# Kernel optimization log

Measured on AMD Instinct MI355X. Metric: run time of the kernel, lower is better.

Reference implementation:

```python
import jax, jax.numpy as jnp
import numpy as np

NUM_NODES = 50000
NUM_RELS = 256
D = 256            # node_in_feat
TEXT_D = 256       # text_emb_dim
T_TOTAL = 24       # number of unique timestep graphs
E = 20000          # edges per timestep graph
B = 16             # batch of query times
SEQ_LEN = 7


def setup_inputs() -> dict:
    key = jax.random.key(0)
    ks = jax.random.split(key, 12)
    s = 1.0 / np.sqrt(D)
    return {
        "node_embeds": jax.random.normal(ks[0], (NUM_NODES, D), jnp.float32),
        "text_emb": jax.random.normal(ks[1], (T_TOTAL, E, TEXT_D), jnp.float32),
        "text_w_W": jax.random.uniform(ks[2], (TEXT_D, D), jnp.float32, -s, s),
        "text_w_b": jax.random.uniform(ks[3], (D,), jnp.float32, -s, s),
        "edge_w_W": jax.random.uniform(ks[4], (3 * D, D), jnp.float32, -s, s),
        "edge_w_b": jax.random.uniform(ks[5], (D,), jnp.float32, -s, s),
        "gru_Wih": jax.random.uniform(ks[6], (D, 3 * D), jnp.float32, -s, s),
        "gru_Whh": jax.random.uniform(ks[7], (D, 3 * D), jnp.float32, -s, s),
        "gru_bih": jax.random.uniform(ks[8], (3 * D,), jnp.float32, -s, s),
        "gru_bhh": jax.random.uniform(ks[9], (3 * D,), jnp.float32, -s, s),
        "edge_src": jax.random.randint(ks[10], (T_TOTAL, E), 0, NUM_NODES, jnp.int32),
        "edge_dst": jax.random.randint(jax.random.fold_in(ks[10], 1), (T_TOTAL, E), 0, NUM_NODES, jnp.int32),
        "edge_rel": jax.random.randint(jax.random.fold_in(ks[10], 2), (T_TOTAL, E), 0, NUM_RELS, jnp.int32),
        "time_idx": jax.random.randint(ks[11], (B, SEQ_LEN), 0, T_TOTAL, jnp.int32),
    }


def _gru(seqs, Wih, Whh, bih, bhh):
    # seqs: [B, R, S, d] -> run GRU over S, return final hidden [B, R, d]
    xs = jnp.moveaxis(seqs, 2, 0)  # [S, B, R, d]
    h0 = jnp.zeros(seqs.shape[:2] + (seqs.shape[-1],), seqs.dtype)

    def step(h, x):
        gi = x @ Wih + bih            # [B, R, 3d]
        gh = h @ Whh + bhh
        i_r, i_z, i_n = jnp.split(gi, 3, axis=-1)
        h_r, h_z, h_n = jnp.split(gh, 3, axis=-1)
        r = jax.nn.sigmoid(i_r + h_r)
        z = jax.nn.sigmoid(i_z + h_z)
        n = jnp.tanh(i_n + r * h_n)
        h_new = (1.0 - z) * n + z * h
        return h_new, None

    h_final, _ = jax.lax.scan(step, h0, xs)
    return h_final


def reference(node_embeds, text_emb, text_w_W, text_w_b, edge_w_W, edge_w_b,
              gru_Wih, gru_Whh, gru_bih, gru_bhh,
              edge_src, edge_dst, edge_rel, time_idx):
    # edge text projection (text_w): [T, E, D]
    text_h = text_emb @ text_w_W + text_w_b
    # gather node embeddings per edge endpoint
    h_src = node_embeds[edge_src]  # [T, E, D]
    h_dst = node_embeds[edge_dst]  # [T, E, D]
    # concat + edge MLP + ReLU: e_h = relu(edge_w([src || text || dst]))
    e = jnp.concatenate([h_src, text_h, h_dst], axis=-1)  # [T, E, 3D]
    e_h = jax.nn.relu(e @ edge_w_W + edge_w_b)            # [T, E, D]

    # scatter-mean of edge embeddings by relation type per timestep graph;
    # relations absent in a graph get zeros (init_rel_embeds = zeros)
    seg = lambda v, r: jax.ops.segment_sum(v, r, num_segments=NUM_RELS)
    sums = jax.vmap(seg)(e_h, edge_rel)                               # [T, R, D]
    counts = jax.vmap(seg)(jnp.ones(edge_rel.shape, e_h.dtype), edge_rel)  # [T, R]
    counts = counts[..., None]
    rel_emb = jnp.where(counts > 0, sums / jnp.maximum(counts, 1.0), 0.0)  # [T, R, D]

    # per query time: gather its window of timestep rel-embeddings and run
    # the GRU over time (relations act as the GRU batch dim, like transpose(0,1))
    seqs = rel_emb[time_idx]                 # [B, S, R, D]
    seqs = jnp.swapaxes(seqs, 1, 2)          # [B, R, S, D]
    hn = _gru(seqs, gru_Wih, gru_Whh, gru_bih, gru_bhh)  # [B, R, D]
    return hn
```

## Files before the change

### kernel.cpp

```cpp
#include <hip/hip_runtime.h>
#include <cstdint>
#include <cstddef>

#define NNODES 50000
#define NPAD   50048
#define NRELS  256
#define DIM    256
#define TT     24
#define EE     20000
#define BATCH  16
#define SEQQ   7

typedef __bf16 bf16;
typedef __bf16 bf16x4 __attribute__((ext_vector_type(4)));
typedef __bf16 bf16x8 __attribute__((ext_vector_type(8)));
typedef float  f32x4  __attribute__((ext_vector_type(4)));

__device__ __forceinline__ void gload16(const void* g, void* l){
  __builtin_amdgcn_global_load_lds((const __attribute__((address_space(1))) void*)g,
                                   (__attribute__((address_space(3))) void*)l, 16, 0, 0);
}


__global__ void k_cvt8(const float* __restrict__ in, bf16* __restrict__ out, int n8){
  int i = blockIdx.x*256 + threadIdx.x;
  if (i >= n8) return;
  const float4* p = (const float4*)in + (size_t)i*2;
  float4 a = p[0], b = p[1];
  bf16x8 o;
  o[0]=(bf16)a.x; o[1]=(bf16)a.y; o[2]=(bf16)a.z; o[3]=(bf16)a.w;
  o[4]=(bf16)b.x; o[5]=(bf16)b.y; o[6]=(bf16)b.z; o[7]=(bf16)b.w;
  ((bf16x8*)out)[i] = o;
}

__global__ void k_build_wbt(const float* __restrict__ tW, const float* __restrict__ eW,
                            bf16* __restrict__ WbT){
  int n = blockIdx.x, j = threadIdx.x;
  WbT[(size_t)n*768 + j]       = (bf16)eW[(size_t)j*256 + n];
  WbT[(size_t)n*768 + 512 + j] = (bf16)eW[(size_t)(512+j)*256 + n];
  float acc = 0.f;
  for (int m=0; m<256; ++m) acc += tW[(size_t)j*256 + m] * eW[(size_t)(256+m)*256 + n];
  WbT[(size_t)n*768 + 256 + j] = (bf16)acc;
}

__global__ void k_bias(const float* __restrict__ tb, const float* __restrict__ eW,
                       const float* __restrict__ eb, float* __restrict__ bf){
  int n = threadIdx.x;
  float acc = eb[n];
  for (int m=0; m<256; ++m) acc += tb[m] * eW[(size_t)(256+m)*256 + n];
  bf[n] = acc;
}

__global__ void k_gruWT(const float* __restrict__ W, bf16* __restrict__ WT){
  int n = blockIdx.x, k = threadIdx.x;
  WT[(size_t)n*256 + k] = (bf16)W[(size_t)k*768 + n];
}

__global__ void k_hist(const int* __restrict__ rel, int* __restrict__ counts,
                       int* __restrict__ offs, int* __restrict__ cursor){
  __shared__ int hist[256];
  __shared__ int scan[256];
  int t = blockIdx.x, tid = threadIdx.x;
  hist[tid] = 0;
  __syncthreads();
  for (int e = tid; e < EE; e += 256) atomicAdd(&hist[rel[(size_t)t*EE + e]], 1);
  __syncthreads();
  int v = hist[tid];
  scan[tid] = v;
  __syncthreads();
  for (int d=1; d<256; d<<=1){
    int add = (tid >= d) ? scan[tid-d] : 0;
    __syncthreads();
    scan[tid] += add;
    __syncthreads();
  }
  int ex = scan[tid] - v;
  counts[t*256+tid] = v;
  offs[t*256+tid]   = ex;
  cursor[t*256+tid] = ex;
}

__global__ void k_perm(const int* __restrict__ rel, const int* __restrict__ esrc,
                       const int* __restrict__ edst, int* __restrict__ cursor,
                       int* __restrict__ gperm, int* __restrict__ src_p,
                       int* __restrict__ dst_p){
  int t = blockIdx.y;
  int e = blockIdx.x*256 + threadIdx.x;
  if (e < EE){
    int r = rel[(size_t)t*EE + e];
    int p = atomicAdd(&cursor[t*256 + r], 1);
    size_t g = (size_t)t*EE + p;
    gperm[g] = t*EE + e;
    src_p[g] = esrc[(size_t)t*EE + e];
    dst_p[g] = edst[(size_t)t*EE + e];
  }
}

__global__ __launch_bounds__(256) void k_projn(
    const bf16* __restrict__ Abf, const bf16* __restrict__ WbT, int koff,
    bf16* __restrict__ out)
{
  int m0 = blockIdx.x*128;
  int tid = threadIdx.x, lane = tid&63, w = tid>>6;
  int l15 = lane&15, lq = lane>>4;
  int c0 = w*64;
  __shared__ __align__(16) bf16 Al[128*32];
  __shared__ __align__(16) bf16 Bl[256*32];

  f32x4 acc[8][4];
  f32x4 z4 = {0.f,0.f,0.f,0.f};
  #pragma unroll
  for (int mi=0;mi<8;++mi)
    #pragma unroll
    for (int ni=0;ni<4;++ni) acc[mi][ni]=z4;

  for (int ks=0; ks<8; ++ks){
    int k0 = ks*32;
    #pragma unroll
    for (int p=0;p<2;++p){
      int c = p*256 + tid;
      int rw = c>>2, prt = c&3;
      int pp = prt ^ ((rw>>1)&3);
      const char* src = (const char*)(Abf + (size_t)(m0+rw)*256 + k0) + pp*16;
      gload16(src, (char*)Al + (size_t)(p*256 + w*64)*16);
    }
    #pragma unroll
    for (int p=0;p<4;++p){
      int c = p*256 + tid;
      int nn = c>>2, prt = c&3;
      int pp = prt ^ ((nn>>1)&3);
      const char* src = (const char*)(WbT + (size_t)nn*768 + koff + k0) + pp*16;
      gload16(src, (char*)Bl + (size_t)(p*256 + w*64)*16);
    }
    __syncthreads();
    bf16x8 b[4];
    #pragma unroll
    for (int ni=0;ni<4;++ni){
      int nn = c0 + ni*16 + l15;
      b[ni] = *(const bf16x8*)((const char*)Bl + (size_t)nn*64 + (size_t)((lq ^ ((nn>>1)&3))*16));
    }
    #pragma unroll
    for (int mi=0;mi<8;++mi){
      int rw = mi*16 + l15;
      bf16x8 a = *(const bf16x8*)((const char*)Al + (size_t)rw*64 + (size_t)((lq ^ ((rw>>1)&3))*16));
      #pragma unroll
      for (int ni=0;ni<4;++ni)
        acc[mi][ni] = __builtin_amdgcn_mfma_f32_16x16x32_bf16(b[ni], a, acc[mi][ni], 0,0,0);
    }
    __syncthreads();
  }
  #pragma unroll
  for (int mi=0;mi<8;++mi){
    int row = m0 + mi*16 + l15;
    #pragma unroll
    for (int ni=0;ni<4;++ni){
      bf16x4 o;
      #pragma unroll
      for (int q=0;q<4;++q) o[q] = (bf16)acc[mi][ni][q];
      *(bf16x4*)(out + (size_t)row*256 + c0 + ni*16 + lq*4) = o;
    }
  }
}

__global__ __launch_bounds__(256,4) void k_projt(
    const float* __restrict__ text, const int* __restrict__ gperm,
    const bf16* __restrict__ WbT, bf16* __restrict__ out)
{
  int m0 = blockIdx.x*64;
  int tid = threadIdx.x, lane = tid&63, w = tid>>6;
  int l15 = lane&15, lq = lane>>4;
  int c0 = w*64;
  __shared__ __align__(16) bf16 Al[64*32];
  __shared__ __align__(16) bf16 Bl[256*32];

  int r0 = tid>>2;
  int part = tid&3;
  int pp0 = part ^ ((r0>>1)&3);
  const float* aP0 = text + (size_t)gperm[m0 + r0]*256;

  f32x4 acc[4][4];
  f32x4 z4 = {0.f,0.f,0.f,0.f};
  #pragma unroll
  for (int mi=0;mi<4;++mi)
    #pragma unroll
    for (int ni=0;ni<4;++ni) acc[mi][ni]=z4;

  for (int ks=0; ks<8; ++ks){
    int k0 = ks*32;
    {
      const float* sp = aP0 + k0 + pp0*8;
      float4 u = ((const float4*)sp)[0], v = ((const float4*)sp)[1];
      bf16x8 o;
      o[0]=(bf16)u.x; o[1]=(bf16)u.y; o[2]=(bf16)u.z; o[3]=(bf16)u.w;
      o[4]=(bf16)v.x; o[5]=(bf16)v.y; o[6]=(bf16)v.z; o[7]=(bf16)v.w;
      *(bf16x8*)((char*)Al + (size_t)tid*16) = o;
    }
    #pragma unroll
    for (int p=0;p<4;++p){
      int c = p*256 + tid;
      int nn = c>>2, prt = c&3;
      int pp = prt ^ ((nn>>1)&3);
      const char* src = (const char*)(WbT + (size_t)nn*768 + 256 + k0) + pp*16;
      gload16(src, (char*)Bl + (size_t)(p*256 + w*64)*16);
    }
    __syncthreads();
    bf16x8 b[4];
    #pragma unroll
    for (int ni=0;ni<4;++ni){
      int nn = c0 + ni*16 + l15;
      b[ni] = *(const bf16x8*)((const char*)Bl + (size_t)nn*64 + (size_t)((lq ^ ((nn>>1)&3))*16));
    }
    #pragma unroll
    for (int mi=0;mi<4;++mi){
      int rw = mi*16 + l15;
      bf16x8 a = *(const bf16x8*)((const char*)Al + (size_t)rw*64 + (size_t)((lq ^ ((rw>>1)&3))*16));
      #pragma unroll
      for (int ni=0;ni<4;++ni)
        acc[mi][ni] = __builtin_amdgcn_mfma_f32_16x16x32_bf16(b[ni], a, acc[mi][ni], 0,0,0);
    }
    __syncthreads();
  }
  #pragma unroll
  for (int mi=0;mi<4;++mi){
    int row = m0 + mi*16 + l15;
    #pragma unroll
    for (int ni=0;ni<4;++ni){
      bf16x4 o;
      #pragma unroll
      for (int q=0;q<4;++q) o[q] = (bf16)acc[mi][ni][q];
      *(bf16x4*)(out + (size_t)row*256 + c0 + ni*16 + lq*4) = o;
    }
  }
}

__global__ __launch_bounds__(256) void k_comb(
    const bf16* __restrict__ P, const bf16* __restrict__ Q,
    const bf16* __restrict__ T, const float* __restrict__ bfused,
    const int* __restrict__ src_p, const int* __restrict__ dst_p,
    const int* __restrict__ counts, const int* __restrict__ offs,
    bf16* __restrict__ rel_bf)
{
  int r = blockIdx.x, t = blockIdx.y;
  int tid = threadIdx.x;
  int tr = t*256 + r;
  int nE = counts[tr];
  if (nE == 0){
    rel_bf[(size_t)tr*256 + tid] = (bf16)0.f;
    return;
  }
  int base = offs[tr];
  int es = tid>>5, cg = (tid&31)*8;
  float bb[8];
  {
    float4 b0 = *(const float4*)(bfused + cg);
    float4 b1 = *(const float4*)(bfused + cg + 4);
    bb[0]=b0.x; bb[1]=b0.y; bb[2]=b0.z; bb[3]=b0.w;
    bb[4]=b1.x; bb[5]=b1.y; bb[6]=b1.z; bb[7]=b1.w;
  }
  float acc[8];
  #pragma unroll
  for (int j=0;j<8;++j) acc[j]=0.f;
  for (int i = es; i < nE; i += 8){
    size_t g = (size_t)t*EE + base + i;
    int s = src_p[g], d = dst_p[g];
    bf16x8 pv = *(const bf16x8*)(P + (size_t)s*256 + cg);
    bf16x8 qv = *(const bf16x8*)(Q + (size_t)d*256 + cg);
    bf16x8 tv = *(const bf16x8*)(T + g*256 + cg);
    #pragma unroll
    for (int j=0;j<8;++j)
      acc[j] += fmaxf((float)pv[j] + (float)qv[j] + (float)tv[j] + bb[j], 0.f);
  }
  __shared__ float red[8][256];
  #pragma unroll
  for (int j=0;j<8;++j) red[es][cg+j] = acc[j];
  __syncthreads();
  float s = 0.f;
  #pragma unroll
  for (int e=0;e<8;++e) s += red[e][tid];
  rel_bf[(size_t)tr*256 + tid] = (bf16)(s / (float)nE);
}

__global__ __launch_bounds__(256) void k_gemm(
    const bf16* __restrict__ A, const bf16* __restrict__ BT,
    const float* __restrict__ bias, float* __restrict__ Out)
{
  int m0 = blockIdx.x*128, n0 = blockIdx.y*128;
  int tid = threadIdx.x, lane = tid&63, w = tid>>6;
  int l15 = lane&15, lq = lane>>4;
  __shared__ __align__(16) bf16 Al[128*32];
  __shared__ __align__(16) bf16 Bl[128*32];
  int wr = (w&1)*64, wc = (w>>1)*64;
  f32x4 acc[4][4];
  f32x4 z4 = {0.f,0.f,0.f,0.f};
  #pragma unroll
  for (int mi=0;mi<4;++mi)
    #pragma unroll
    for (int ni=0;ni<4;++ni) acc[mi][ni]=z4;
  for (int ks=0; ks<8; ++ks){
    int k0 = ks*32;
    #pragma unroll
    for (int p=0;p<2;++p){
      int c = p*256 + tid;
      int rw = c>>2, part = c&3;
      int pp = part ^ ((rw>>1)&3);
      const char* src = (const char*)(A + (size_t)(m0+rw)*256 + k0) + pp*16;
      gload16(src, (char*)Al + (size_t)(p*256 + w*64)*16);
    }
    #pragma unroll
    for (int p=0;p<2;++p){
      int c = p*256 + tid;
      int nn = c>>2, part = c&3;
      int pp = part ^ ((nn>>1)&3);
      const char* src = (const char*)(BT + (size_t)(n0+nn)*256 + k0) + pp*16;
      gload16(src, (char*)Bl + (size_t)(p*256 + w*64)*16);
    }
    __syncthreads();
    bf16x8 a[4], b[4];
    #pragma unroll
    for (int mi=0;mi<4;++mi){
      int rw = wr + mi*16 + l15;
      a[mi] = *(const bf16x8*)((const char*)Al + (size_t)rw*64 + (size_t)((lq ^ ((rw>>1)&3))*16));
    }
    #pragma unroll
    for (int ni=0;ni<4;++ni){
      int nn = wc + ni*16 + l15;
      b[ni] = *(const bf16x8*)((const char*)Bl + (size_t)nn*64 + (size_t)((lq ^ ((nn>>1)&3))*16));
    }
    #pragma unroll
    for (int mi=0;mi<4;++mi)
      #pragma unroll
      for (int ni=0;ni<4;++ni)
        acc[mi][ni] = __builtin_amdgcn_mfma_f32_16x16x32_bf16(a[mi], b[ni], acc[mi][ni], 0,0,0);
    __syncthreads();
  }
  #pragma unroll
  for (int ni=0;ni<4;++ni){
    int col = n0 + wc + ni*16 + l15;
    float bv = bias[col];
    #pragma unroll
    for (int mi=0;mi<4;++mi){
      #pragma unroll
      for (int q=0;q<4;++q){
        int row = m0 + wr + mi*16 + lq*4 + q;
        Out[(size_t)row*768 + col] = acc[mi][ni][q] + bv;
      }
    }
  }
}

__global__ void k_update(const float* __restrict__ GI, const float* __restrict__ gh,
                         const float* __restrict__ bhh, const int* __restrict__ time_idx,
                         const float* __restrict__ h_in, float* __restrict__ h_out,
                         bf16* __restrict__ hbf_out, float* __restrict__ out_final, int s)
{
  int row = blockIdx.x;
  int d = threadIdx.x;
  int b = row >> 8, rr = row & 255;
  int t = time_idx[b*SEQQ + s];
  size_t gib = (size_t)(t*256 + rr)*768;
  float ir = GI[gib + d], iz = GI[gib + 256 + d], inn = GI[gib + 512 + d];
  float hr, hz, hn;
  if (s == 0){ hr = bhh[d]; hz = bhh[256+d]; hn = bhh[512+d]; }
  else { size_t gb = (size_t)row*768; hr = gh[gb+d]; hz = gh[gb+256+d]; hn = gh[gb+512+d]; }
  float rg = 1.f/(1.f + __expf(-(ir+hr)));
  float zz = 1.f/(1.f + __expf(-(iz+hz)));
  float nn = tanhf(inn + rg*hn);
  float hp = (s==0) ? 0.f : h_in[(size_t)row*256 + d];
  float hv = (1.f - zz)*nn + zz*hp;
  if (s == SEQQ-1){
    out_final[(size_t)row*256 + d] = hv;
  } else {
    h_out[(size_t)row*256 + d] = hv;
    hbf_out[(size_t)row*256 + d] = (bf16)hv;
  }
}

extern "C" void kernel_launch(void* const* d_in, const int* in_sizes, int n_in,
                              void* d_out, int out_size, void* d_ws, size_t ws_size,
                              hipStream_t stream)
{
  (void)in_sizes; (void)n_in; (void)out_size; (void)ws_size;
  const float* node_embeds = (const float*)d_in[0];
  const float* text_emb    = (const float*)d_in[1];
  const float* text_w_W    = (const float*)d_in[2];
  const float* text_w_b    = (const float*)d_in[3];
  const float* edge_w_W    = (const float*)d_in[4];
  const float* edge_w_b    = (const float*)d_in[5];
  const float* gru_Wih     = (const float*)d_in[6];
  const float* gru_Whh     = (const float*)d_in[7];
  const float* gru_bih     = (const float*)d_in[8];
  const float* gru_bhh     = (const float*)d_in[9];
  const int* edge_src      = (const int*)d_in[10];
  const int* edge_dst      = (const int*)d_in[11];
  const int* edge_rel      = (const int*)d_in[12];
  const int* time_idx      = (const int*)d_in[13];
  float* out = (float*)d_out;
  char* ws = (char*)d_ws;

  size_t o = 0;
  bf16*  WbT    = (bf16*) (ws + o); o += (size_t)768*256*2;
  bf16*  WihT   = (bf16*) (ws + o); o += (size_t)768*256*2;
  bf16*  WhhT   = (bf16*) (ws + o); o += (size_t)768*256*2;
  float* bfused = (float*)(ws + o); o += 1024;
  bf16*  node_bf= (bf16*) (ws + o); o += (size_t)NPAD*256*2;
  int*   counts = (int*)  (ws + o); o += (size_t)TT*256*4;
  int*   offs   = (int*)  (ws + o); o += (size_t)TT*256*4;
  int*   cursor = (int*)  (ws + o); o += (size_t)TT*256*4;
  int*   gperm  = (int*)  (ws + o); o += (size_t)TT*EE*4;
  int*   src_p  = (int*)  (ws + o); o += (size_t)TT*EE*4;
  int*   dst_p  = (int*)  (ws + o); o += (size_t)TT*EE*4;
  bf16*  rel_bf = (bf16*) (ws + o); o += (size_t)TT*256*256*2;
  bf16*  P      = (bf16*) (ws + o); o += (size_t)NPAD*256*2;
  bf16*  Q      = (bf16*) (ws + o); o += (size_t)NPAD*256*2;
  size_t oT = o;
  bf16*  Tproj  = (bf16*) (ws + oT);
  float* GI     = (float*)(ws + oT); size_t o2 = oT + (size_t)TT*256*768*4;
  float* h      = (float*)(ws + o2); o2 += (size_t)4096*256*4;
  bf16*  hbf    = (bf16*) (ws + o2); o2 += (size_t)4096*256*2;
  float* gh     = (float*)(ws + o2); o2 += (size_t)4096*768*4;

  k_cvt8<<<6250,256,0,stream>>>(node_embeds, node_bf, NNODES*256/8);
  k_build_wbt<<<256,256,0,stream>>>(text_w_W, edge_w_W, WbT);
  k_bias<<<1,256,0,stream>>>(text_w_b, edge_w_W, edge_w_b, bfused);
  k_gruWT<<<768,256,0,stream>>>(gru_Wih, WihT);
  k_gruWT<<<768,256,0,stream>>>(gru_Whh, WhhT);
  k_hist<<<TT,256,0,stream>>>(edge_rel, counts, offs, cursor);
  k_perm<<<dim3((EE+255)/256,TT),256,0,stream>>>(edge_rel, edge_src, edge_dst,
                                                 cursor, gperm, src_p, dst_p);
  k_projn<<<NPAD/128,256,0,stream>>>(node_bf, WbT, 0,   P);
  k_projn<<<NPAD/128,256,0,stream>>>(node_bf, WbT, 512, Q);
  k_projt<<<TT*EE/64,256,0,stream>>>(text_emb, gperm, WbT, Tproj);
  k_comb<<<dim3(256,TT),256,0,stream>>>(P, Q, Tproj, bfused, src_p, dst_p,
                                        counts, offs, rel_bf);
  k_gemm<<<dim3(48,6),256,0,stream>>>(rel_bf, WihT, gru_bih, GI);
  for (int s=0; s<SEQQ; ++s){
    if (s > 0)
      k_gemm<<<dim3(32,6),256,0,stream>>>(hbf, WhhT, gru_bhh, gh);
    k_update<<<4096,256,0,stream>>>(GI, gh, gru_bhh, time_idx, h, h, hbf, out, s);
  }
}
```

Measured before the change: 636.9 us.

## Fuse GRU recurrence into one persistent kernel with in-register hidden state

Replaces the per-timestep sequence of Whh GEMM plus elementwise update launches (13 launches) with a single kernel. Each block owns 16 relation rows of one batch element, keeps the hidden state in registers, and stages the bf16 copy in shared memory for the MFMA h@Whh product. This removes launch overhead and the global round-trips of h and gh between steps. In exchange, only 256 blocks run and each streams the whole Whh matrix from global/L2 at every step without LDS tiling, which may limit throughput.

New measurement: 595.1 us. 1.07x faster.

```diff
diff --git a/kernel.cpp b/kernel.cpp
--- a/kernel.cpp
+++ b/kernel.cpp
@@ -348,30 +348,73 @@
   }
 }
 
-__global__ void k_update(const float* __restrict__ GI, const float* __restrict__ gh,
-                         const float* __restrict__ bhh, const int* __restrict__ time_idx,
-                         const float* __restrict__ h_in, float* __restrict__ h_out,
-                         bf16* __restrict__ hbf_out, float* __restrict__ out_final, int s)
-{
-  int row = blockIdx.x;
-  int d = threadIdx.x;
-  int b = row >> 8, rr = row & 255;
-  int t = time_idx[b*SEQQ + s];
-  size_t gib = (size_t)(t*256 + rr)*768;
-  float ir = GI[gib + d], iz = GI[gib + 256 + d], inn = GI[gib + 512 + d];
-  float hr, hz, hn;
-  if (s == 0){ hr = bhh[d]; hz = bhh[256+d]; hn = bhh[512+d]; }
-  else { size_t gb = (size_t)row*768; hr = gh[gb+d]; hz = gh[gb+256+d]; hn = gh[gb+512+d]; }
-  float rg = 1.f/(1.f + __expf(-(ir+hr)));
-  float zz = 1.f/(1.f + __expf(-(iz+hz)));
-  float nn = tanhf(inn + rg*hn);
-  float hp = (s==0) ? 0.f : h_in[(size_t)row*256 + d];
-  float hv = (1.f - zz)*nn + zz*hp;
-  if (s == SEQQ-1){
-    out_final[(size_t)row*256 + d] = hv;
-  } else {
-    h_out[(size_t)row*256 + d] = hv;
-    hbf_out[(size_t)row*256 + d] = (bf16)hv;
+__global__ __launch_bounds__(256) void k_gru(
+    const float* __restrict__ GI, const bf16* __restrict__ WhhT,
+    const float* __restrict__ bhh, const int* __restrict__ time_idx,
+    float* __restrict__ out)
+{
+  int blk = blockIdx.x;
+  int tid = threadIdx.x, lane = tid&63, w = tid>>6;
+  int l15 = lane&15, lq = lane>>4;
+  int b = blk >> 4;
+  int rr = ((blk & 15)*16) + l15;
+  __shared__ __align__(16) bf16 Ah[16*256];
+
+  f32x4 h[4];
+  #pragma unroll
+  for (int jq=0;jq<4;++jq) h[jq] = f32x4{0.f,0.f,0.f,0.f};
+
+  for (int s=0; s<SEQQ; ++s){
+    int t = time_idx[b*SEQQ + s];
+    size_t gib = (size_t)(t*256 + rr)*768;
+    f32x4 gh[12];
+    #pragma unroll
+    for (int ni=0;ni<12;++ni){
+      int col = (ni>>2)*256 + w*64 + (ni&3)*16 + lq*4;
+      gh[ni] = *(const f32x4*)(bhh + col);
+    }
+    if (s > 0){
+      #pragma unroll
+      for (int ks=0; ks<8; ++ks){
+        bf16x8 a = *(const bf16x8*)(&Ah[0] + (size_t)l15*256 + ks*32 + lq*8);
+        #pragma unroll
+        for (int ni=0;ni<12;++ni){
+          int n = (ni>>2)*256 + w*64 + (ni&3)*16 + l15;
+          bf16x8 wv = *(const bf16x8*)(WhhT + (size_t)n*256 + ks*32 + lq*8);
+          gh[ni] = __builtin_amdgcn_mfma_f32_16x16x32_bf16(wv, a, gh[ni], 0,0,0);
+        }
+      }
+    }
+    #pragma unroll
+    for (int jq=0;jq<4;++jq){
+      int col = w*64 + jq*16 + lq*4;
+      f32x4 ir = *(const f32x4*)(GI + gib + col);
+      f32x4 iz = *(const f32x4*)(GI + gib + 256 + col);
+      f32x4 in = *(const f32x4*)(GI + gib + 512 + col);
+      #pragma unroll
+      for (int q=0;q<4;++q){
+        float rg = 1.f/(1.f + __expf(-(ir[q] + gh[jq][q])));
+        float zz = 1.f/(1.f + __expf(-(iz[q] + gh[4+jq][q])));
+        float nn = tanhf(in[q] + rg*gh[8+jq][q]);
+        h[jq][q] = (1.f - zz)*nn + zz*h[jq][q];
+      }
+    }
+    if (s < SEQQ-1){
+      __syncthreads();
+      #pragma unroll
+      for (int jq=0;jq<4;++jq){
+        bf16x4 o;
+        #pragma unroll
+        for (int q=0;q<4;++q) o[q] = (bf16)h[jq][q];
+        *(bf16x4*)(&Ah[0] + (size_t)l15*256 + w*64 + jq*16 + lq*4) = o;
+      }
+      __syncthreads();
+    }
+  }
+  #pragma unroll
+  for (int jq=0;jq<4;++jq){
+    f32x4 o = h[jq];
+    *(f32x4*)(out + (size_t)(blk*16 + l15)*256 + w*64 + jq*16 + lq*4) = o;
   }
 }
 
@@ -414,10 +457,7 @@
   bf16*  Q      = (bf16*) (ws + o); o += (size_t)NPAD*256*2;
   size_t oT = o;
   bf16*  Tproj  = (bf16*) (ws + oT);
-  float* GI     = (float*)(ws + oT); size_t o2 = oT + (size_t)TT*256*768*4;
-  float* h      = (float*)(ws + o2); o2 += (size_t)4096*256*4;
-  bf16*  hbf    = (bf16*) (ws + o2); o2 += (size_t)4096*256*2;
-  float* gh     = (float*)(ws + o2); o2 += (size_t)4096*768*4;
+  float* GI     = (float*)(ws + oT);
 
   k_cvt8<<<6250,256,0,stream>>>(node_embeds, node_bf, NNODES*256/8);
   k_build_wbt<<<256,256,0,stream>>>(text_w_W, edge_w_W, WbT);
@@ -433,9 +473,5 @@
   k_comb<<<dim3(256,TT),256,0,stream>>>(P, Q, Tproj, bfused, src_p, dst_p,
                                         counts, offs, rel_bf);
   k_gemm<<<dim3(48,6),256,0,stream>>>(rel_bf, WihT, gru_bih, GI);
-  for (int s=0; s<SEQQ; ++s){
-    if (s > 0)
-      k_gemm<<<dim3(32,6),256,0,stream>>>(hbf, WhhT, gru_bhh, gh);
-    k_update<<<4096,256,0,stream>>>(GI, gh, gru_bhh, time_idx, h, h, hbf, out, s);
-  }
-}
+  k_gru<<<256,256,0,stream>>>(GI, WhhT, gru_bhh, time_idx, out);
+}
```
